# Optimization experiments

Hardware: AMD Instinct MI355X
Metric: run time of the kernel (lower is better)

## Reference

```python
import jax, jax.numpy as jnp
import numpy as np

N_NODES = 50000
N_EDGES = 800000
IN_DIM = 128
OUT_DIM = 128
CLASS_NUM = 40
EPS = 0.0  # PyG GINConv default eps


def setup_inputs() -> dict:
    key = jax.random.key(0)
    k1, k2, k3, k4 = jax.random.split(key, 4)
    x = jax.random.normal(k1, (N_NODES, IN_DIM), dtype=jnp.float32)
    edge_index = jax.random.randint(k2, (2, N_EDGES), 0, N_NODES, dtype=jnp.int64)
    # Linear(in, out, bias=False) weights, torch layout [out, in]
    W1 = jax.random.normal(k3, (OUT_DIM, IN_DIM), dtype=jnp.float32) / np.sqrt(IN_DIM)
    W2 = jax.random.normal(k4, (CLASS_NUM, OUT_DIM), dtype=jnp.float32) / np.sqrt(OUT_DIM)
    return {"x": x, "edge_index": edge_index, "W1": W1, "W2": W2}


def gin_conv(x, edge_index, W):
    # GINConv: nn((1+eps)*x + sum_{j in N(i)} x_j)
    src, dst = edge_index[0], edge_index[1]
    agg = jax.ops.segment_sum(x[src], dst, num_segments=x.shape[0])  # [N, d]
    h = (1.0 + EPS) * x + agg
    return h @ W.T


def reference(x, edge_index, W1, W2):
    # Layer 1 + relu (dropout is identity at inference, p=0.5 only in training)
    h = jax.nn.relu(gin_conv(x, edge_index, W1))
    # Layer 2 (logits)
    out = gin_conv(h, edge_index, W2)
    return out
```

## Files before the change

### kernel.cpp

```cpp
#include <hip/hip_runtime.h>

#define N_NODES 50000
#define N_EDGES 800000
#define BSHIFT 7
#define BKT_NODES 128
#define NBKT   ((N_NODES + BKT_NODES - 1) >> BSHIFT)
#define CAP    4096
#define CHUNK_EDGES 8192
#define NBIN_BLOCKS ((N_EDGES + CHUNK_EDGES - 1) / CHUNK_EDGES)
#define NPERM  (NBKT * BKT_NODES)
#define NB32P  (NPERM / 32)
#define N_PAD  50048
#define GEMM1_NB ((N_NODES + 63) / 64)

typedef __attribute__((ext_vector_type(8))) short short8;
typedef __attribute__((ext_vector_type(4))) float f32x4;
typedef __attribute__((ext_vector_type(2))) float f32x2;

__device__ __forceinline__ int load_idx(const void* ei, int is64, long long pos) {
  return is64 ? (int)((const long long*)ei)[pos] : ((const int*)ei)[pos];
}

__device__ __forceinline__ unsigned bfr(float f) {
  unsigned u = __float_as_uint(f);
  return (u + 0x7FFFu + ((u >> 16) & 1u)) >> 16;
}
__device__ __forceinline__ unsigned bfpk(float lo, float hi) {
  return bfr(lo) | (bfr(hi) << 16);
}
#define ACC_BF4F(acc, u)                                                   \
  acc.x += __uint_as_float((u).x << 16);                                   \
  acc.y += __uint_as_float((u).x);                                         \
  acc.z += __uint_as_float((u).y << 16);                                   \
  acc.w += __uint_as_float((u).y);

#define ACC_FP8(a0, a1, u) {                                               \
  f32x2 t0 = __builtin_amdgcn_cvt_pk_f32_fp8((int)(u).x, false);           \
  f32x2 t1 = __builtin_amdgcn_cvt_pk_f32_fp8((int)(u).x, true);            \
  f32x2 t2 = __builtin_amdgcn_cvt_pk_f32_fp8((int)(u).y, false);           \
  f32x2 t3 = __builtin_amdgcn_cvt_pk_f32_fp8((int)(u).y, true);            \
  a0.x += t0.x; a0.y += t0.y; a0.z += t1.x; a0.w += t1.y;                  \
  a1.x += t2.x; a1.y += t2.y; a1.z += t3.x; a1.w += t3.y; }

__global__ __launch_bounds__(256) void prep_kernel(const float* __restrict__ W1,
                                                   const float* __restrict__ W2,
                                                   int* __restrict__ resv,
                                                   unsigned short* __restrict__ W1bf,
                                                   unsigned short* __restrict__ W2bf) {
  int b = blockIdx.x, tid = threadIdx.x;
  if (b == 0) {
    ((int4*)resv)[tid] = make_int4(0, 0, 0, 0);
    return;
  }
  int j = (b - 1) * 256 + tid;
  if (j < 128 * 128) {
    W1bf[j] = (unsigned short)bfr(W1[j]);
  } else {
    int jj = j - 128 * 128;
    int c = jj >> 7, k = jj & 127;
    W2bf[jj] = (c < 40) ? (unsigned short)bfr(W2[c * 128 + k]) : 0;
  }
}

__global__ __launch_bounds__(256) void binGemm1_kernel(const void* __restrict__ ei,
                                                       int* __restrict__ resv,
                                                       unsigned* __restrict__ binned,
                                                       const float* __restrict__ xin,
                                                       const unsigned short* __restrict__ W1bf,
                                                       unsigned char* __restrict__ Ysfp) {
  __shared__ unsigned short Ysh[64 * 128];
  __shared__ int cnt[NBKT];
  __shared__ int lbase[NBKT];
  __shared__ int sflag;
  int tid = threadIdx.x;

  if (blockIdx.x < NBIN_BLOCKS) {
    if (tid < 64) {
      const long long* e64 = (const long long*)ei;
      long long v = e64[tid];
      unsigned long long m = __ballot(v >= 0 && v < N_NODES);
      if (tid == 0) sflag = (m == ~0ull) ? 1 : 0;
    }
    for (int i = tid; i < NBKT; i += 256) cnt[i] = 0;
    __syncthreads();
    int f = sflag;
    long long base = (long long)blockIdx.x * CHUNK_EDGES;
    unsigned pk[CHUNK_EDGES / 256];
    #pragma unroll
    for (int it = 0; it < CHUNK_EDGES / 256; ++it) {
      long long e = base + it * 256 + tid;
      unsigned p = 0xFFFFFFFFu;
      if (e < N_EDGES) {
        int src = load_idx(ei, f, e);
        int dst = load_idx(ei, f, (long long)N_EDGES + e);
        int bk = dst >> BSHIFT;
        p = (unsigned)src | ((unsigned)(dst & 127) << 16) | ((unsigned)bk << 23);
        atomicAdd(&cnt[bk], 1);
      }
      pk[it] = p;
    }
    __syncthreads();
    for (int i = tid; i < NBKT; i += 256) {
      int c = cnt[i];
      lbase[i] = c ? (i * CAP + atomicAdd(&resv[i], c)) : 0;
      cnt[i] = 0;
    }
    __syncthreads();
    #pragma unroll
    for (int it = 0; it < CHUNK_EDGES / 256; ++it) {
      unsigned p = pk[it];
      if (p != 0xFFFFFFFFu) {
        int bk = p >> 23;
        int off = atomicAdd(&cnt[bk], 1);
        binned[lbase[bk] + off] = p & 0x7FFFFFu;
      }
    }
    return;
  }

  int wave = tid >> 6, lane = tid & 63;
  int rl = lane & 15, kg = lane >> 4;
  int n0 = (blockIdx.x - NBIN_BLOCKS) * 64;
  int rowg = n0 + wave * 16 + rl;
  int row = (rowg < N_NODES) ? rowg : (N_NODES - 1);
  f32x4 acc[8];
  #pragma unroll
  for (int t = 0; t < 8; ++t) acc[t] = (f32x4)(0.f);
  #pragma unroll
  for (int kk = 0; kk < 4; ++kk) {
    int k0 = kk * 32 + kg * 8;
    const float* xr = xin + (size_t)row * 128 + k0;
    float4 a0 = *(const float4*)xr;
    float4 a1 = *(const float4*)(xr + 4);
    short8 a;
    a[0] = (short)bfr(a0.x); a[1] = (short)bfr(a0.y);
    a[2] = (short)bfr(a0.z); a[3] = (short)bfr(a0.w);
    a[4] = (short)bfr(a1.x); a[5] = (short)bfr(a1.y);
    a[6] = (short)bfr(a1.z); a[7] = (short)bfr(a1.w);
    #pragma unroll
    for (int t = 0; t < 8; ++t) {
      short8 b = *(const short8*)(W1bf + (t * 16 + rl) * 128 + k0);
      acc[t] = __builtin_amdgcn_mfma_f32_16x16x32_bf16(a, b, acc[t], 0, 0, 0);
    }
  }
  #pragma unroll
  for (int t = 0; t < 8; ++t) {
    #pragma unroll
    for (int reg = 0; reg < 4; ++reg)
      Ysh[(wave * 16 + kg * 4 + reg) * 128 + t * 16 + rl] =
          (unsigned short)bfr(acc[t][reg]);
  }
  __syncthreads();
  int rows = N_NODES - n0; if (rows > 64) rows = 64;
  uint2* dstb = (uint2*)Ysfp;
  const unsigned* ysh32 = (const unsigned*)Ysh;
  for (int i = tid; i < rows * 16; i += 256) {
    int r = i >> 4, j = i & 15;
    int base = r * 64 + j * 4;
    unsigned u0 = ysh32[base + 0], u1 = ysh32[base + 1];
    unsigned u2 = ysh32[base + 2], u3 = ysh32[base + 3];
    float d0 = __uint_as_float(u0 << 16), d1 = __uint_as_float(u0 & 0xffff0000u);
    float d2 = __uint_as_float(u1 << 16), d3 = __uint_as_float(u1 & 0xffff0000u);
    float d4 = __uint_as_float(u2 << 16), d5 = __uint_as_float(u2 & 0xffff0000u);
    float d6 = __uint_as_float(u3 << 16), d7 = __uint_as_float(u3 & 0xffff0000u);
    int wx = __builtin_amdgcn_cvt_pk_fp8_f32(d0, d1, 0, false);
    wx = __builtin_amdgcn_cvt_pk_fp8_f32(d2, d3, wx, true);
    int wy = __builtin_amdgcn_cvt_pk_fp8_f32(d4, d5, 0, false);
    wy = __builtin_amdgcn_cvt_pk_fp8_f32(d6, d7, wy, true);
    int slice = j >> 3, cs = j & 7;
    dstb[(size_t)slice * (N_PAD * 8) + (size_t)(n0 + r) * 8 + cs] =
        make_uint2((unsigned)wx, (unsigned)wy);
  }
}

__global__ __launch_bounds__(256) void csr_kernel(const unsigned* __restrict__ binned,
                                                  const int* __restrict__ resv,
                                                  unsigned short* __restrict__ col,
                                                  uint2* __restrict__ permInfo) {
  __shared__ int red[256];
  __shared__ int ncnt[BKT_NODES];
  __shared__ int ncur[BKT_NODES];
  __shared__ int dcnt[64];
  __shared__ int dcur[64];
  int tid = threadIdx.x;
  int b = blockIdx.x;
  int s = 0;
  for (int i = tid; i < b; i += 256) s += resv[i];
  red[tid] = s;
  __syncthreads();
  #pragma unroll
  for (int off = 128; off > 0; off >>= 1) {
    if (tid < off) red[tid] += red[tid + off];
    __syncthreads();
  }
  int gb = red[0];
  int c = resv[b];
  if (tid < BKT_NODES) ncnt[tid] = 0;
  if (tid < 64) dcnt[tid] = 0;
  if (tid < BKT_NODES) permInfo[(size_t)b * BKT_NODES + tid] = make_uint2(0u, 0xFFFFu);
  __syncthreads();
  const unsigned* bb = binned + (size_t)b * CAP;
  for (int i = tid; i < c; i += 256)
    atomicAdd(&ncnt[(bb[i] >> 16) & 127], 1);
  __syncthreads();
  if (tid == 0) {
    int a = gb;
    #pragma unroll
    for (int j = 0; j < BKT_NODES; ++j) { int t = ncnt[j]; ncur[j] = a; a += t; }
  }
  __syncthreads();
  int node0 = b << BSHIFT;
  int nvalid = N_NODES - node0; if (nvalid > BKT_NODES) nvalid = BKT_NODES;
  int mystart = 0, mydeg = 0;
  if (tid < nvalid) {
    mystart = ncur[tid];
    mydeg = ncnt[tid];
    int db = mydeg > 63 ? 63 : mydeg;
    atomicAdd(&dcnt[db], 1);
  }
  __syncthreads();
  if (tid == 0) {
    int a = 0;
    #pragma unroll
    for (int j = 0; j < 64; ++j) { int t = dcnt[j]; dcur[j] = a; a += t; }
  }
  __syncthreads();
  if (tid < nvalid) {
    int db = mydeg > 63 ? 63 : mydeg;
    int rank = atomicAdd(&dcur[db], 1);
    permInfo[(size_t)b * BKT_NODES + rank] =
        make_uint2((unsigned)mystart,
                   (unsigned)(node0 + tid) | ((unsigned)mydeg << 16));
  }
  __syncthreads();
  for (int i = tid; i < c; i += 256) {
    unsigned p = bb[i];
    int slot = atomicAdd(&ncur[(p >> 16) & 127], 1);
    col[slot] = (unsigned short)(p & 0xFFFFu);
  }
}

__global__ __launch_bounds__(256) void gather1_kernel(const unsigned char* __restrict__ Ysfp,
                                                      const unsigned short* __restrict__ col,
                                                      const uint2* __restrict__ permInfo,
                                                      unsigned short* __restrict__ h1bf) {
  int bid = blockIdx.x;
  int slice = bid / NB32P;
  int nb = bid - slice * NB32P;
  int lane = threadIdx.x & 63;
  int wv = threadIdx.x >> 6;
  int g = lane >> 3, s = lane & 7;
  int slot = nb * 32 + wv * 8 + g;
  uint2 pi = permInfo[slot];
  int node = pi.y & 0xFFFFu;
  if (node == 0xFFFF) return;
  int i = (int)pi.x;
  int end = i + (int)(pi.y >> 16);
  const uint2* Y2 = (const uint2*)(Ysfp + (size_t)slice * N_PAD * 64);
  float4 a0 = make_float4(0.f, 0.f, 0.f, 0.f);
  float4 a1 = make_float4(0.f, 0.f, 0.f, 0.f);
  {
    uint2 u = Y2[(size_t)node * 8 + s];
    ACC_FP8(a0, a1, u);
  }
  for (; i + 3 < end; i += 4) {
    int s0 = col[i], s1 = col[i + 1], s2 = col[i + 2], s3 = col[i + 3];
    uint2 u0 = Y2[(size_t)s0 * 8 + s];
    uint2 u1 = Y2[(size_t)s1 * 8 + s];
    uint2 u2 = Y2[(size_t)s2 * 8 + s];
    uint2 u3 = Y2[(size_t)s3 * 8 + s];
    ACC_FP8(a0, a1, u0); ACC_FP8(a0, a1, u1);
    ACC_FP8(a0, a1, u2); ACC_FP8(a0, a1, u3);
  }
  for (; i < end; ++i) {
    uint2 u = Y2[(size_t)col[i] * 8 + s];
    ACC_FP8(a0, a1, u);
  }
  uint4 p;
  p.x = bfpk(fmaxf(a0.x, 0.f), fmaxf(a0.y, 0.f));
  p.y = bfpk(fmaxf(a0.z, 0.f), fmaxf(a0.w, 0.f));
  p.z = bfpk(fmaxf(a1.x, 0.f), fmaxf(a1.y, 0.f));
  p.w = bfpk(fmaxf(a1.z, 0.f), fmaxf(a1.w, 0.f));
  ((uint4*)h1bf)[(size_t)node * 16 + slice * 8 + s] = p;
}

__global__ __launch_bounds__(256) void gather2_kernel(const unsigned short* __restrict__ Zbf,
                                                      const unsigned short* __restrict__ col,
                                                      const uint2* __restrict__ permInfo,
                                                      float* __restrict__ outp) {
  int lane = threadIdx.x & 63;
  int wv = threadIdx.x >> 6;
  int g = lane >> 3, s = lane & 7;
  int slot = blockIdx.x * 32 + wv * 8 + g;
  uint2 pi = permInfo[slot];
  int node = pi.y & 0xFFFFu;
  if (node == 0xFFFF) return;
  int i = (int)pi.x;
  int end = i + (int)(pi.y >> 16);
  const uint2* Z2 = (const uint2*)Zbf;
  bool ex = s < 2;
  float4 acc = make_float4(0.f, 0.f, 0.f, 0.f);
  float4 acc2 = make_float4(0.f, 0.f, 0.f, 0.f);
  {
    uint2 u = Z2[(size_t)node * 10 + s];
    ACC_BF4F(acc, u);
    if (ex) { uint2 v = Z2[(size_t)node * 10 + 8 + s]; ACC_BF4F(acc2, v); }
  }
  for (; i + 1 < end; i += 2) {
    int s0 = col[i], s1 = col[i + 1];
    uint2 u0 = Z2[(size_t)s0 * 10 + s];
    uint2 u1 = Z2[(size_t)s1 * 10 + s];
    ACC_BF4F(acc, u0); ACC_BF4F(acc, u1);
    if (ex) {
      uint2 v0 = Z2[(size_t)s0 * 10 + 8 + s];
      uint2 v1 = Z2[(size_t)s1 * 10 + 8 + s];
      ACC_BF4F(acc2, v0); ACC_BF4F(acc2, v1);
    }
  }
  for (; i < end; ++i) {
    int s0 = col[i];
    uint2 u0 = Z2[(size_t)s0 * 10 + s];
    ACC_BF4F(acc, u0);
    if (ex) { uint2 v0 = Z2[(size_t)s0 * 10 + 8 + s]; ACC_BF4F(acc2, v0); }
  }
  float4* o4 = (float4*)(outp + (size_t)node * 40);
  o4[s] = acc;
  if (ex) o4[8 + s] = acc2;
}

__global__ __launch_bounds__(256) void gemm2_kernel(const unsigned short* __restrict__ h1bf,
                                                    const unsigned short* __restrict__ W2bf,
                                                    unsigned short* __restrict__ Zbf) {
  __shared__ unsigned short Zsh[64 * 40];
  int tid = threadIdx.x;
  int wave = tid >> 6, lane = tid & 63;
  int rl = lane & 15, kg = lane >> 4;
  int n0 = blockIdx.x * 64;
  int rowg = n0 + wave * 16 + rl;
  int row = (rowg < N_NODES) ? rowg : (N_NODES - 1);
  f32x4 acc[3];
  #pragma unroll
  for (int t = 0; t < 3; ++t) acc[t] = (f32x4)(0.f);
  #pragma unroll
  for (int kk = 0; kk < 4; ++kk) {
    int k0 = kk * 32 + kg * 8;
    short8 a = *(const short8*)(h1bf + (size_t)row * 128 + k0);
    #pragma unroll
    for (int t = 0; t < 3; ++t) {
      short8 b = *(const short8*)(W2bf + (t * 16 + rl) * 128 + k0);
      acc[t] = __builtin_amdgcn_mfma_f32_16x16x32_bf16(a, b, acc[t], 0, 0, 0);
    }
  }
  #pragma unroll
  for (int t = 0; t < 3; ++t) {
    int c = t * 16 + rl;
    if (c < 40) {
      #pragma unroll
      for (int reg = 0; reg < 4; ++reg)
        Zsh[(wave * 16 + kg * 4 + reg) * 40 + c] = (unsigned short)bfr(acc[t][reg]);
    }
  }
  __syncthreads();
  int rows = N_NODES - n0; if (rows > 64) rows = 64;
  unsigned* dst = (unsigned*)Zbf + (size_t)n0 * 20;
  const unsigned* src = (const unsigned*)Zsh;
  for (int i = tid; i < rows * 20; i += 256) dst[i] = src[i];
}

extern "C" void kernel_launch(void* const* d_in, const int* in_sizes, int n_in,
                              void* d_out, int out_size, void* d_ws, size_t ws_size,
                              hipStream_t stream) {
  const float* x  = (const float*)d_in[0];
  const void*  ei = d_in[1];
  const float* W1 = (const float*)d_in[2];
  const float* W2 = (const float*)d_in[3];
  float* out = (float*)d_out;

  int* resv   = (int*)d_ws;
  unsigned* binned = (unsigned*)(resv + 1024);
  unsigned short* col = (unsigned short*)(binned + (size_t)NBKT * CAP);
  uint2* permInfo = (uint2*)(col + N_EDGES);
  unsigned char* Ysfp = (unsigned char*)(permInfo + NPERM);
  unsigned short* h1bf = (unsigned short*)(Ysfp + (size_t)2 * N_PAD * 64);
  unsigned short* W1bf = h1bf + (size_t)N_NODES * 128;
  unsigned short* W2bf = W1bf + 128 * 128;
  unsigned short* Zbf  = (unsigned short*)Ysfp;

  prep_kernel<<<89, 256, 0, stream>>>(W1, W2, resv, W1bf, W2bf);
  binGemm1_kernel<<<NBIN_BLOCKS + GEMM1_NB, 256, 0, stream>>>(ei, resv, binned,
                                                              x, W1bf, Ysfp);
  csr_kernel<<<NBKT, 256, 0, stream>>>(binned, resv, col, permInfo);
  gather1_kernel<<<2 * NB32P, 256, 0, stream>>>(Ysfp, col, permInfo, h1bf);
  gemm2_kernel<<<GEMM1_NB, 256, 0, stream>>>(h1bf, W2bf, Zbf);
  gather2_kernel<<<NB32P, 256, 0, stream>>>(Zbf, col, permInfo, out);
}
```

Measured before the change: 96.89 us.

## Fuse CSR construction with first-layer gather using shared-memory column lists

Merges the CSR build and the layer-1 gather into one kernel per 128-node bucket. The bucket's column indices and permutation info stay in shared memory, so the gather reads neighbor indices from LDS instead of global memory, and one kernel launch plus a global round trip go away. The global col and permInfo arrays are still written for the second gather. In exchange, parallelism falls: the fused kernel runs only NBKT (~391) blocks, each handling both feature slices and four passes serially, where the old gather used about 3.1k blocks. It also needs roughly 8KB more LDS per block.

```diff
diff --git a/kernel.cpp b/kernel.cpp
--- a/kernel.cpp
+++ b/kernel.cpp
@@ -173,10 +173,14 @@
   }
 }
 
-__global__ __launch_bounds__(256) void csr_kernel(const unsigned* __restrict__ binned,
-                                                  const int* __restrict__ resv,
-                                                  unsigned short* __restrict__ col,
-                                                  uint2* __restrict__ permInfo) {
+__global__ __launch_bounds__(256) void csrGather1_kernel(const unsigned* __restrict__ binned,
+                                                         const int* __restrict__ resv,
+                                                         unsigned short* __restrict__ col,
+                                                         uint2* __restrict__ permInfo,
+                                                         const unsigned char* __restrict__ Ysfp,
+                                                         unsigned short* __restrict__ h1bf) {
+  __shared__ unsigned short colL[CAP];
+  __shared__ uint2 pinfoL[BKT_NODES];
   __shared__ int red[256];
   __shared__ int ncnt[BKT_NODES];
   __shared__ int ncur[BKT_NODES];
@@ -184,6 +188,7 @@
   __shared__ int dcur[64];
   int tid = threadIdx.x;
   int b = blockIdx.x;
+
   int s = 0;
   for (int i = tid; i < b; i += 256) s += resv[i];
   red[tid] = s;
@@ -195,16 +200,19 @@
   }
   int gb = red[0];
   int c = resv[b];
-  if (tid < BKT_NODES) ncnt[tid] = 0;
+  if (tid < BKT_NODES) {
+    ncnt[tid] = 0;
+    pinfoL[tid] = make_uint2(0u, 0xFFFFu);
+    permInfo[(size_t)b * BKT_NODES + tid] = make_uint2(0u, 0xFFFFu);
+  }
   if (tid < 64) dcnt[tid] = 0;
-  if (tid < BKT_NODES) permInfo[(size_t)b * BKT_NODES + tid] = make_uint2(0u, 0xFFFFu);
   __syncthreads();
   const unsigned* bb = binned + (size_t)b * CAP;
   for (int i = tid; i < c; i += 256)
     atomicAdd(&ncnt[(bb[i] >> 16) & 127], 1);
   __syncthreads();
   if (tid == 0) {
-    int a = gb;
+    int a = 0;
     #pragma unroll
     for (int j = 0; j < BKT_NODES; ++j) { int t = ncnt[j]; ncur[j] = a; a += t; }
   }
@@ -228,60 +236,61 @@
   if (tid < nvalid) {
     int db = mydeg > 63 ? 63 : mydeg;
     int rank = atomicAdd(&dcur[db], 1);
-    permInfo[(size_t)b * BKT_NODES + rank] =
-        make_uint2((unsigned)mystart,
-                   (unsigned)(node0 + tid) | ((unsigned)mydeg << 16));
+    unsigned nd = (unsigned)(node0 + tid) | ((unsigned)mydeg << 16);
+    pinfoL[rank] = make_uint2((unsigned)mystart, nd);
+    permInfo[(size_t)b * BKT_NODES + rank] = make_uint2((unsigned)(gb + mystart), nd);
   }
   __syncthreads();
   for (int i = tid; i < c; i += 256) {
     unsigned p = bb[i];
     int slot = atomicAdd(&ncur[(p >> 16) & 127], 1);
-    col[slot] = (unsigned short)(p & 0xFFFFu);
-  }
-}
-
-__global__ __launch_bounds__(256) void gather1_kernel(const unsigned char* __restrict__ Ysfp,
-                                                      const unsigned short* __restrict__ col,
-                                                      const uint2* __restrict__ permInfo,
-                                                      unsigned short* __restrict__ h1bf) {
-  int bid = blockIdx.x;
-  int slice = bid / NB32P;
-  int nb = bid - slice * NB32P;
-  int lane = threadIdx.x & 63;
-  int wv = threadIdx.x >> 6;
-  int g = lane >> 3, s = lane & 7;
-  int slot = nb * 32 + wv * 8 + g;
-  uint2 pi = permInfo[slot];
-  int node = pi.y & 0xFFFFu;
-  if (node == 0xFFFF) return;
-  int i = (int)pi.x;
-  int end = i + (int)(pi.y >> 16);
-  const uint2* Y2 = (const uint2*)(Ysfp + (size_t)slice * N_PAD * 64);
-  float4 a0 = make_float4(0.f, 0.f, 0.f, 0.f);
-  float4 a1 = make_float4(0.f, 0.f, 0.f, 0.f);
-  {
-    uint2 u = Y2[(size_t)node * 8 + s];
-    ACC_FP8(a0, a1, u);
-  }
-  for (; i + 3 < end; i += 4) {
-    int s0 = col[i], s1 = col[i + 1], s2 = col[i + 2], s3 = col[i + 3];
-    uint2 u0 = Y2[(size_t)s0 * 8 + s];
-    uint2 u1 = Y2[(size_t)s1 * 8 + s];
-    uint2 u2 = Y2[(size_t)s2 * 8 + s];
-    uint2 u3 = Y2[(size_t)s3 * 8 + s];
-    ACC_FP8(a0, a1, u0); ACC_FP8(a0, a1, u1);
-    ACC_FP8(a0, a1, u2); ACC_FP8(a0, a1, u3);
-  }
-  for (; i < end; ++i) {
-    uint2 u = Y2[(size_t)col[i] * 8 + s];
-    ACC_FP8(a0, a1, u);
-  }
-  uint4 p;
-  p.x = bfpk(fmaxf(a0.x, 0.f), fmaxf(a0.y, 0.f));
-  p.y = bfpk(fmaxf(a0.z, 0.f), fmaxf(a0.w, 0.f));
-  p.z = bfpk(fmaxf(a1.x, 0.f), fmaxf(a1.y, 0.f));
-  p.w = bfpk(fmaxf(a1.z, 0.f), fmaxf(a1.w, 0.f));
-  ((uint4*)h1bf)[(size_t)node * 16 + slice * 8 + s] = p;
+    unsigned short sv = (unsigned short)(p & 0xFFFFu);
+    colL[slot] = sv;
+    col[gb + slot] = sv;
+  }
+  __syncthreads();
+
+  int grp = (tid & 63) >> 3;
+  int wv = tid >> 6;
+  int s8 = tid & 7;
+  int gidx = wv * 8 + grp;
+  #pragma unroll
+  for (int slice = 0; slice < 2; ++slice) {
+    const uint2* Y2 = (const uint2*)(Ysfp + (size_t)slice * N_PAD * 64);
+    #pragma unroll
+    for (int pass = 0; pass < 4; ++pass) {
+      uint2 pi = pinfoL[pass * 32 + gidx];
+      int node = pi.y & 0xFFFFu;
+      if (node == 0xFFFF) continue;
+      int i = (int)pi.x;
+      int end = i + (int)(pi.y >> 16);
+      float4 a0 = make_float4(0.f, 0.f, 0.f, 0.f);
+      float4 a1 = make_float4(0.f, 0.f, 0.f, 0.f);
+      {
+        uint2 u = Y2[(size_t)node * 8 + s8];
+        ACC_FP8(a0, a1, u);
+      }
+      for (; i + 3 < end; i += 4) {
+        int s0 = colL[i], s1 = colL[i + 1], s2 = colL[i + 2], s3 = colL[i + 3];
+        uint2 u0 = Y2[(size_t)s0 * 8 + s8];
+        uint2 u1 = Y2[(size_t)s1 * 8 + s8];
+        uint2 u2 = Y2[(size_t)s2 * 8 + s8];
+        uint2 u3 = Y2[(size_t)s3 * 8 + s8];
+        ACC_FP8(a0, a1, u0); ACC_FP8(a0, a1, u1);
+        ACC_FP8(a0, a1, u2); ACC_FP8(a0, a1, u3);
+      }
+      for (; i < end; ++i) {
+        uint2 u = Y2[(size_t)colL[i] * 8 + s8];
+        ACC_FP8(a0, a1, u);
+      }
+      uint4 p;
+      p.x = bfpk(fmaxf(a0.x, 0.f), fmaxf(a0.y, 0.f));
+      p.y = bfpk(fmaxf(a0.z, 0.f), fmaxf(a0.w, 0.f));
+      p.z = bfpk(fmaxf(a1.x, 0.f), fmaxf(a1.y, 0.f));
+      p.w = bfpk(fmaxf(a1.z, 0.f), fmaxf(a1.w, 0.f));
+      ((uint4*)h1bf)[(size_t)node * 16 + slice * 8 + s8] = p;
+    }
+  }
 }
 
 __global__ __launch_bounds__(256) void gather2_kernel(const unsigned short* __restrict__ Zbf,
@@ -389,8 +398,8 @@
   prep_kernel<<<89, 256, 0, stream>>>(W1, W2, resv, W1bf, W2bf);
   binGemm1_kernel<<<NBIN_BLOCKS + GEMM1_NB, 256, 0, stream>>>(ei, resv, binned,
                                                               x, W1bf, Ysfp);
-  csr_kernel<<<NBKT, 256, 0, stream>>>(binned, resv, col, permInfo);
-  gather1_kernel<<<2 * NB32P, 256, 0, stream>>>(Ysfp, col, permInfo, h1bf);
+  csrGather1_kernel<<<NBKT, 256, 0, stream>>>(binned, resv, col, permInfo,
+                                              Ysfp, h1bf);
   gemm2_kernel<<<GEMM1_NB, 256, 0, stream>>>(h1bf, W2bf, Zbf);
   gather2_kernel<<<NB32P, 256, 0, stream>>>(Zbf, col, permInfo, out);
 }
```

After: 101.1 us. +4.3%, slower.
